# Optimization experiments

Hardware: AMD Instinct MI355X
Metric: run time of the kernel (lower is better)

## Reference

```python
import jax, jax.numpy as jnp
import numpy as np

B, S, D = 2, 400, 512  # batch, seq (src == tgt for self-attention), dim; attn_hidden=0 so d == D


def setup_inputs() -> dict:
    key = jax.random.key(0)
    ks = jax.random.split(key, 9)
    inv = 1.0 / np.sqrt(D)
    return {
        "input": jax.random.normal(ks[0], (B, S, D), jnp.float32),
        "memory_bank": jax.random.normal(ks[1], (B, S, D), jnp.float32),
        # lengths in [S//2, S], guaranteed >= 2 so no row is fully masked
        "memory_lengths": jax.random.randint(ks[2], (B,), S // 2, S + 1, jnp.int32),
        "Wq": jax.random.normal(ks[3], (D, D), jnp.float32) * inv,   # linear_query.weight^T
        "bq": jax.random.normal(ks[4], (D,), jnp.float32) * inv,      # linear_query.bias
        "Wc": jax.random.normal(ks[5], (D, D), jnp.float32) * inv,   # linear_context.weight^T
        "v": jax.random.normal(ks[6], (D,), jnp.float32) * inv,       # v.weight (d -> 1)
        "Wout": jax.random.normal(ks[7], (2 * D, D), jnp.float32) * inv,  # linear_out.weight^T
        "bout": jax.random.normal(ks[8], (D,), jnp.float32) * inv,
    }


def reference(input, memory_bank, memory_lengths, Wq, bq, Wc, v, Wout, bout):
    b, s, d = memory_bank.shape
    # Bahdanau/mlp score: v^T tanh(Wq q + b + Wc h)
    wq = jnp.einsum("btd,de->bte", input, Wq) + bq            # [B,T,d]
    uh = jnp.einsum("bsd,de->bse", memory_bank, Wc)           # [B,S,d]
    wquh = jnp.tanh(wq[:, :, None, :] + uh[:, None, :, :])    # [B,T,S,d] big intermediate
    scores = jnp.einsum("btse,e->bts", wquh, v)               # [B,T,S]
    # padding mask (j < length) with self position masked out on the diagonal
    pos = jnp.arange(s)
    key_mask = pos[None, :] < memory_lengths[:, None]         # [B,S]
    mask = key_mask[:, None, :] & (pos[:, None] != pos[None, :])  # [B,T,S]
    scores = jnp.where(mask, scores, -jnp.inf)
    align = jax.nn.softmax(scores, axis=2)                    # [B,T,S]
    c = jnp.einsum("bts,bsd->btd", align, memory_bank)        # context [B,T,D]
    concat_c = jnp.concatenate([c, input], axis=2)            # [B,T,2D]
    attn_h = jnp.einsum("btf,fd->btd", concat_c, Wout) + bout # [B,T,D]
    # mlp variant: no sigmoid gating
    return attn_h.transpose(1, 0, 2), align.transpose(1, 0, 2)  # [T,B,D], [T,B,S]
```

## Files before the change

kernel.cpp:

```cpp
#include <hip/hip_runtime.h>
#include <math.h>

#define BB 2
#define SS 400
#define DD 512
#define TWO_LOG2E 2.8853900817779268f

#if __has_builtin(__builtin_amdgcn_exp2f)
#define EXP2F(x) __builtin_amdgcn_exp2f(x)
#else
#define EXP2F(x) exp2f(x)
#endif
#define RCPF(x) __builtin_amdgcn_rcpf(x)

#define EAOFF 0
#define MOFF 409600
#define EB4OFF 819200
#define XOFF 1228800

typedef __bf16 bf16x8 __attribute__((ext_vector_type(8)));
typedef float floatx16 __attribute__((ext_vector_type(16)));

__global__ __launch_bounds__(256) void k0_all(
    const float* __restrict__ Wq, const float* __restrict__ Wc,
    const float* __restrict__ Wout, const float* __restrict__ input,
    const float* __restrict__ mbk, unsigned short* __restrict__ wt,
    unsigned short* __restrict__ ahi, unsigned short* __restrict__ alo)
{
    const int gid = blockIdx.x;
    if (gid < 1024) {
        const int g   = gid >> 9;
        const int rem = gid & 511;
        const int k0  = (rem & 15) * 32;
        const int n0  = (rem >> 4) * 32;

        __shared__ float tile[32][33];
        const int nn  = threadIdx.x & 31;
        const int kk0 = threadIdx.x >> 5;
        const int n   = n0 + nn;

        #pragma unroll
        for (int p = 0; p < 4; ++p) {
            const int k = k0 + kk0 + p * 8;
            float val;
            if (n0 < 512) val = (g ? Wc : Wq)[(size_t)k * 512 + n];
            else          val = Wout[((size_t)(g ? k : 512 + k)) * 512 + (n - 512)];
            tile[kk0 + p * 8][nn] = val;
        }
        __syncthreads();

        const int kc = threadIdx.x & 31;
        #pragma unroll
        for (int p = 0; p < 4; ++p) {
            const int nl = (threadIdx.x >> 5) + p * 8;
            const __bf16 h = (__bf16)tile[kc][nl];
            wt[((size_t)(g * 1024 + n0 + nl)) * 512 + k0 + kc] =
                __builtin_bit_cast(unsigned short, h);
        }
    } else {
        const int cid = gid - 1024;
        const int g   = (cid >= 400) ? 1 : 0;
        const int i4  = (cid - g * 400) * 256 + threadIdx.x;
        const float4 a = ((const float4*)(g ? mbk : input))[i4];
        ushort4 h, l;
        #pragma unroll
        for (int j = 0; j < 4; ++j) {
            const float av = (&a.x)[j];
            const __bf16 hh = (__bf16)av;
            (&h.x)[j] = __builtin_bit_cast(unsigned short, hh);
            const __bf16 ll = (__bf16)(av - (float)hh);
            (&l.x)[j] = __builtin_bit_cast(unsigned short, ll);
        }
        ((ushort4*)(ahi + (size_t)g * 409600))[i4] = h;
        ((ushort4*)(alo + (size_t)g * 409600))[i4] = l;
    }
}

__global__ __launch_bounds__(64) void k1_mfma(
    const unsigned short* __restrict__ ahi, const unsigned short* __restrict__ alo,
    const unsigned short* __restrict__ wt, const float* __restrict__ bq,
    const float* __restrict__ bout, float* __restrict__ ws,
    float* __restrict__ out0)
{
    const int lane = threadIdx.x;
    const int mt   = blockIdx.x;
    const int np   = blockIdx.y;
    const int g    = blockIdx.z;
    const int m    = lane & 31;
    const int kh   = lane >> 5;
    const int n0   = np * 64;

    const size_t arow = ((size_t)g * 800 + mt * 32 + m) * 512 + kh * 8;
    const unsigned short* __restrict__ ah = ahi + arow;
    const unsigned short* __restrict__ al = alo + arow;
    const unsigned short* __restrict__ w0 =
        wt + ((size_t)(g * 1024 + n0 + m)) * 512 + kh * 8;
    const unsigned short* __restrict__ w1 = w0 + (size_t)32 * 512;

    floatx16 acc0h, acc0l, acc1h, acc1l;
    #pragma unroll
    for (int i = 0; i < 16; ++i) { acc0h[i] = 0.f; acc0l[i] = 0.f;
                                   acc1h[i] = 0.f; acc1l[i] = 0.f; }

    #pragma unroll 4
    for (int ks = 0; ks < 32; ++ks) {
        const bf16x8 va0 = *(const bf16x8*)(ah + ks * 16);
        const bf16x8 va1 = *(const bf16x8*)(al + ks * 16);
        const bf16x8 bh0 = *(const bf16x8*)(w0 + ks * 16);
        const bf16x8 bh1 = *(const bf16x8*)(w1 + ks * 16);

        acc0h = __builtin_amdgcn_mfma_f32_32x32x16_bf16(va0, bh0, acc0h, 0, 0, 0);
        acc0l = __builtin_amdgcn_mfma_f32_32x32x16_bf16(va1, bh0, acc0l, 0, 0, 0);
        acc1h = __builtin_amdgcn_mfma_f32_32x32x16_bf16(va0, bh1, acc1h, 0, 0, 0);
        acc1l = __builtin_amdgcn_mfma_f32_32x32x16_bf16(va1, bh1, acc1l, 0, 0, 0);
    }

    const floatx16 c0 = acc0h + acc0l;
    const floatx16 c1 = acc1h + acc1l;
    const int rbase = kh * 4;

    #pragma unroll
    for (int r = 0; r < 16; ++r) {
        const int row  = (r & 3) + 8 * (r >> 2) + rbase;
        const int grow = mt * 32 + row;
        const int bi   = (grow >= SS) ? 1 : 0;
        const int rl   = grow - bi * SS;
        #pragma unroll
        for (int u = 0; u < 2; ++u) {
            const float val  = u ? c1[r] : c0[r];
            const int   gcol = n0 + u * 32 + m;
            if (g == 0) {
                if (gcol < 512) {
                    ws[EAOFF + (size_t)grow * 512 + gcol] =
                        EXP2F(TWO_LOG2E * (val + bq[gcol]));
                } else {
                    const int d = gcol - 512;
                    out0[((size_t)(rl * BB + bi)) * 512 + d] = val + bout[d];
                }
            } else {
                if (gcol < 512) {
                    ws[EB4OFF + (size_t)((bi * 128 + (gcol >> 2)) * SS + rl) * 4
                       + (gcol & 3)] = EXP2F(TWO_LOG2E * val);
                } else {
                    ws[MOFF + (size_t)grow * 512 + (gcol - 512)] = val;
                }
            }
        }
    }
}

__global__ __launch_bounds__(512) void k2_attn(
    const float* __restrict__ ws, const float* __restrict__ v,
    const int* __restrict__ lens, float* __restrict__ out1,
    float* __restrict__ out0)
{
    const int tp = blockIdx.x;
    const int b  = blockIdx.y;
    const int t0 = tp * 2;
    const int t1 = t0 + 1;
    const int tid = threadIdx.x;
    const int s   = tid;
    const int sidx = (s < SS) ? s : 0;
    const int len  = lens[b];

    __shared__ float lal[SS][2];
    __shared__ float wred0[8], wred1[8];

    const float* __restrict__ ea0p = ws + EAOFF + (size_t)(b * SS + t0) * 512;
    const float* __restrict__ ea1p = ea0p + 512;

    const float4* __restrict__ eb4 =
        (const float4*)(ws + EB4OFF) + (size_t)b * 128 * SS + sidx;

    float acc0 = 0.f, acc1 = 0.f;
    #pragma unroll 4
    for (int e4 = 0; e4 < 128; ++e4) {
        const float4 eb  = eb4[(size_t)e4 * SS];
        const float4 vv  = *(const float4*)(v    + e4 * 4);
        const float4 ea0 = *(const float4*)(ea0p + e4 * 4);
        const float4 ea1 = *(const float4*)(ea1p + e4 * 4);
        {
            const float d0 = fmaf(ea0.x, eb.x, 1.f);
            const float d1 = fmaf(ea0.y, eb.y, 1.f);
            const float d2 = fmaf(ea0.z, eb.z, 1.f);
            const float d3 = fmaf(ea0.w, eb.w, 1.f);
            const float d01 = d0 * d1, d23 = d2 * d3;
            const float n01 = fmaf(vv.x, d1, vv.y * d0);
            const float n23 = fmaf(vv.z, d3, vv.w * d2);
            const float num = fmaf(n01, d23, n23 * d01);
            acc0 = fmaf(num, RCPF(d01 * d23), acc0);
        }
        {
            const float d0 = fmaf(ea1.x, eb.x, 1.f);
            const float d1 = fmaf(ea1.y, eb.y, 1.f);
            const float d2 = fmaf(ea1.z, eb.z, 1.f);
            const float d3 = fmaf(ea1.w, eb.w, 1.f);
            const float d01 = d0 * d1, d23 = d2 * d3;
            const float n01 = fmaf(vv.x, d1, vv.y * d0);
            const float n23 = fmaf(vv.z, d3, vv.w * d2);
            const float num = fmaf(n01, d23, n23 * d01);
            acc1 = fmaf(num, RCPF(d01 * d23), acc1);
        }
    }

    const bool v0 = (s < SS) && (s < len) && (s != t0);
    const bool v1 = (s < SS) && (s < len) && (s != t1);
    const float sc0 = v0 ? -2.f * acc0 : -INFINITY;
    const float sc1 = v1 ? -2.f * acc1 : -INFINITY;

    const int wid  = tid >> 6;
    const int lane = tid & 63;

    float m0 = sc0, m1 = sc1;
    #pragma unroll
    for (int off = 32; off > 0; off >>= 1) {
        m0 = fmaxf(m0, __shfl_xor(m0, off));
        m1 = fmaxf(m1, __shfl_xor(m1, off));
    }
    if (lane == 0) { wred0[wid] = m0; wred1[wid] = m1; }
    __syncthreads();
    float mx0 = wred0[0], mx1 = wred1[0];
    #pragma unroll
    for (int w = 1; w < 8; ++w) {
        mx0 = fmaxf(mx0, wred0[w]);
        mx1 = fmaxf(mx1, wred1[w]);
    }
    __syncthreads();

    const float p0 = v0 ? __expf(sc0 - mx0) : 0.f;
    const float p1 = v1 ? __expf(sc1 - mx1) : 0.f;
    float s0v = p0, s1v = p1;
    #pragma unroll
    for (int off = 32; off > 0; off >>= 1) {
        s0v += __shfl_xor(s0v, off);
        s1v += __shfl_xor(s1v, off);
    }
    if (lane == 0) { wred0[wid] = s0v; wred1[wid] = s1v; }
    __syncthreads();
    float tot0 = wred0[0], tot1 = wred1[0];
    #pragma unroll
    for (int w = 1; w < 8; ++w) { tot0 += wred0[w]; tot1 += wred1[w]; }
    const float inv0 = RCPF(tot0);
    const float inv1 = RCPF(tot1);

    if (s < SS) {
        const float a0 = p0 * inv0;
        const float a1 = p1 * inv1;
        out1[((size_t)(t0 * BB) + b) * SS + s] = a0;
        out1[((size_t)(t1 * BB) + b) * SS + s] = a1;
        lal[s][0] = a0;
        lal[s][1] = a1;
    }
    __syncthreads();

    const float* __restrict__ Mb = ws + MOFF + (size_t)b * SS * DD;
    const int d = tid;
    float c0a = 0.f, c0b = 0.f, c1a = 0.f, c1b = 0.f;
    #pragma unroll 4
    for (int sp = 0; sp < SS; sp += 2) {
        const float mv0 = Mb[(size_t)sp * DD + d];
        const float mv1 = Mb[(size_t)(sp + 1) * DD + d];
        const float2 a0 = *(const float2*)&lal[sp][0];
        const float2 a1 = *(const float2*)&lal[sp + 1][0];
        c0a = fmaf(a0.x, mv0, c0a);
        c1a = fmaf(a0.y, mv0, c1a);
        c0b = fmaf(a1.x, mv1, c0b);
        c1b = fmaf(a1.y, mv1, c1b);
    }
    const size_t o0 = ((size_t)(t0 * BB) + b) * DD + d;
    const size_t o1 = ((size_t)(t1 * BB) + b) * DD + d;
    out0[o0] += c0a + c0b;
    out0[o1] += c1a + c1b;
}

extern "C" void kernel_launch(void* const* d_in, const int* in_sizes, int n_in,
                              void* d_out, int out_size, void* d_ws, size_t ws_size,
                              hipStream_t stream)
{
    const float* input = (const float*)d_in[0];
    const float* mbk   = (const float*)d_in[1];
    const int*   lens  = (const int*)d_in[2];
    const float* Wq    = (const float*)d_in[3];
    const float* bq    = (const float*)d_in[4];
    const float* Wc    = (const float*)d_in[5];
    const float* v     = (const float*)d_in[6];
    const float* Wout  = (const float*)d_in[7];
    const float* bout  = (const float*)d_in[8];

    float* out0 = (float*)d_out;
    float* out1 = out0 + (size_t)BB * SS * DD;
    float* ws   = (float*)d_ws;
    unsigned short* x16 = (unsigned short*)(ws + XOFF);
    unsigned short* wt  = x16;
    unsigned short* ahi = x16 + 1048576;
    unsigned short* alo = ahi + 819200;

    hipLaunchKernelGGL(k0_all, dim3(1824), dim3(256), 0, stream,
                       Wq, Wc, Wout, input, mbk, wt, ahi, alo);
    hipLaunchKernelGGL(k1_mfma, dim3(25, 16, 2), dim3(64), 0, stream,
                       ahi, alo, wt, bq, bout, ws, out0);
    hipLaunchKernelGGL(k2_attn, dim3(200, 2), dim3(512), 0, stream,
                       ws, v, lens, out1, out0);
}
```

Baseline: 145.0 us.

## Split attention score and context reductions across two half-blocks of threads

The attention kernel grows to 1024 threads. Two groups of 512 threads each compute half of the feature dimension of the score, and the partial sums are combined through shared memory. Score work is skipped for key positions at or beyond the sequence length, and the context accumulation only loops up to the length, with its s-range also split between the two halves. This raises parallelism per block and removes padded work, at the cost of extra barriers, more shared memory and tighter register pressure under the 1024-thread launch bound.

New measurement: 155.2 us. +7.0%, slower.

```diff
diff --git a/kernel.cpp b/kernel.cpp
--- a/kernel.cpp
+++ b/kernel.cpp
@@ -149,7 +149,7 @@
     }
 }
 
-__global__ __launch_bounds__(512) void k2_attn(
+__global__ __launch_bounds__(1024, 2) void k2_attn(
     const float* __restrict__ ws, const float* __restrict__ v,
     const int* __restrict__ lens, float* __restrict__ out1,
     float* __restrict__ out0)
@@ -159,12 +159,14 @@
     const int t0 = tp * 2;
     const int t1 = t0 + 1;
     const int tid = threadIdx.x;
-    const int s   = tid;
+    const int h   = tid >> 9;
+    const int s   = tid & 511;
     const int sidx = (s < SS) ? s : 0;
     const int len  = lens[b];
 
+    __shared__ float pacc[2][512];
     __shared__ float lal[SS][2];
-    __shared__ float wred0[8], wred1[8];
+    __shared__ float wredm0[8], wredm1[8], wreds0[8], wreds1[8];
 
     const float* __restrict__ ea0p = ws + EAOFF + (size_t)(b * SS + t0) * 512;
     const float* __restrict__ ea1p = ea0p + 512;
@@ -173,91 +175,109 @@
         (const float4*)(ws + EB4OFF) + (size_t)b * 128 * SS + sidx;
 
     float acc0 = 0.f, acc1 = 0.f;
-    #pragma unroll 4
-    for (int e4 = 0; e4 < 128; ++e4) {
-        const float4 eb  = eb4[(size_t)e4 * SS];
-        const float4 vv  = *(const float4*)(v    + e4 * 4);
-        const float4 ea0 = *(const float4*)(ea0p + e4 * 4);
-        const float4 ea1 = *(const float4*)(ea1p + e4 * 4);
-        {
-            const float d0 = fmaf(ea0.x, eb.x, 1.f);
-            const float d1 = fmaf(ea0.y, eb.y, 1.f);
-            const float d2 = fmaf(ea0.z, eb.z, 1.f);
-            const float d3 = fmaf(ea0.w, eb.w, 1.f);
-            const float d01 = d0 * d1, d23 = d2 * d3;
-            const float n01 = fmaf(vv.x, d1, vv.y * d0);
-            const float n23 = fmaf(vv.z, d3, vv.w * d2);
-            const float num = fmaf(n01, d23, n23 * d01);
-            acc0 = fmaf(num, RCPF(d01 * d23), acc0);
-        }
-        {
-            const float d0 = fmaf(ea1.x, eb.x, 1.f);
-            const float d1 = fmaf(ea1.y, eb.y, 1.f);
-            const float d2 = fmaf(ea1.z, eb.z, 1.f);
-            const float d3 = fmaf(ea1.w, eb.w, 1.f);
-            const float d01 = d0 * d1, d23 = d2 * d3;
-            const float n01 = fmaf(vv.x, d1, vv.y * d0);
-            const float n23 = fmaf(vv.z, d3, vv.w * d2);
-            const float num = fmaf(n01, d23, n23 * d01);
-            acc1 = fmaf(num, RCPF(d01 * d23), acc1);
-        }
-    }
-
-    const bool v0 = (s < SS) && (s < len) && (s != t0);
-    const bool v1 = (s < SS) && (s < len) && (s != t1);
-    const float sc0 = v0 ? -2.f * acc0 : -INFINITY;
-    const float sc1 = v1 ? -2.f * acc1 : -INFINITY;
+    if (s < len) {
+        const int e4b = h * 64;
+        #pragma unroll 4
+        for (int e4 = e4b; e4 < e4b + 64; ++e4) {
+            const float4 eb  = eb4[(size_t)e4 * SS];
+            const float4 vv  = *(const float4*)(v    + e4 * 4);
+            const float4 ea0 = *(const float4*)(ea0p + e4 * 4);
+            const float4 ea1 = *(const float4*)(ea1p + e4 * 4);
+            {
+                const float d0 = fmaf(ea0.x, eb.x, 1.f);
+                const float d1 = fmaf(ea0.y, eb.y, 1.f);
+                const float d2 = fmaf(ea0.z, eb.z, 1.f);
+                const float d3 = fmaf(ea0.w, eb.w, 1.f);
+                const float d01 = d0 * d1, d23 = d2 * d3;
+                const float n01 = fmaf(vv.x, d1, vv.y * d0);
+                const float n23 = fmaf(vv.z, d3, vv.w * d2);
+                const float num = fmaf(n01, d23, n23 * d01);
+                acc0 = fmaf(num, RCPF(d01 * d23), acc0);
+            }
+            {
+                const float d0 = fmaf(ea1.x, eb.x, 1.f);
+                const float d1 = fmaf(ea1.y, eb.y, 1.f);
+                const float d2 = fmaf(ea1.z, eb.z, 1.f);
+                const float d3 = fmaf(ea1.w, eb.w, 1.f);
+                const float d01 = d0 * d1, d23 = d2 * d3;
+                const float n01 = fmaf(vv.x, d1, vv.y * d0);
+                const float n23 = fmaf(vv.z, d3, vv.w * d2);
+                const float num = fmaf(n01, d23, n23 * d01);
+                acc1 = fmaf(num, RCPF(d01 * d23), acc1);
+            }
+        }
+    }
+    if (h == 1) { pacc[0][s] = acc0; pacc[1][s] = acc1; }
+    __syncthreads();
 
     const int wid  = tid >> 6;
     const int lane = tid & 63;
 
-    float m0 = sc0, m1 = sc1;
-    #pragma unroll
-    for (int off = 32; off > 0; off >>= 1) {
-        m0 = fmaxf(m0, __shfl_xor(m0, off));
-        m1 = fmaxf(m1, __shfl_xor(m1, off));
-    }
-    if (lane == 0) { wred0[wid] = m0; wred1[wid] = m1; }
-    __syncthreads();
-    float mx0 = wred0[0], mx1 = wred1[0];
-    #pragma unroll
-    for (int w = 1; w < 8; ++w) {
-        mx0 = fmaxf(mx0, wred0[w]);
-        mx1 = fmaxf(mx1, wred1[w]);
-    }
-    __syncthreads();
-
-    const float p0 = v0 ? __expf(sc0 - mx0) : 0.f;
-    const float p1 = v1 ? __expf(sc1 - mx1) : 0.f;
-    float s0v = p0, s1v = p1;
-    #pragma unroll
-    for (int off = 32; off > 0; off >>= 1) {
-        s0v += __shfl_xor(s0v, off);
-        s1v += __shfl_xor(s1v, off);
-    }
-    if (lane == 0) { wred0[wid] = s0v; wred1[wid] = s1v; }
-    __syncthreads();
-    float tot0 = wred0[0], tot1 = wred1[0];
-    #pragma unroll
-    for (int w = 1; w < 8; ++w) { tot0 += wred0[w]; tot1 += wred1[w]; }
-    const float inv0 = RCPF(tot0);
-    const float inv1 = RCPF(tot1);
-
-    if (s < SS) {
-        const float a0 = p0 * inv0;
-        const float a1 = p1 * inv1;
-        out1[((size_t)(t0 * BB) + b) * SS + s] = a0;
-        out1[((size_t)(t1 * BB) + b) * SS + s] = a1;
-        lal[s][0] = a0;
-        lal[s][1] = a1;
+    bool  v0 = false, v1 = false;
+    float sc0 = -INFINITY, sc1 = -INFINITY;
+    if (h == 0) {
+        acc0 += pacc[0][s];
+        acc1 += pacc[1][s];
+        v0 = (s < SS) && (s < len) && (s != t0);
+        v1 = (s < SS) && (s < len) && (s != t1);
+        sc0 = v0 ? -2.f * acc0 : -INFINITY;
+        sc1 = v1 ? -2.f * acc1 : -INFINITY;
+
+        float m0 = sc0, m1 = sc1;
+        #pragma unroll
+        for (int off = 32; off > 0; off >>= 1) {
+            m0 = fmaxf(m0, __shfl_xor(m0, off));
+            m1 = fmaxf(m1, __shfl_xor(m1, off));
+        }
+        if (lane == 0) { wredm0[wid] = m0; wredm1[wid] = m1; }
+    }
+    __syncthreads();
+
+    float p0 = 0.f, p1 = 0.f;
+    if (h == 0) {
+        float mx0 = wredm0[0], mx1 = wredm1[0];
+        #pragma unroll
+        for (int w = 1; w < 8; ++w) {
+            mx0 = fmaxf(mx0, wredm0[w]);
+            mx1 = fmaxf(mx1, wredm1[w]);
+        }
+        p0 = v0 ? __expf(sc0 - mx0) : 0.f;
+        p1 = v1 ? __expf(sc1 - mx1) : 0.f;
+        float s0v = p0, s1v = p1;
+        #pragma unroll
+        for (int off = 32; off > 0; off >>= 1) {
+            s0v += __shfl_xor(s0v, off);
+            s1v += __shfl_xor(s1v, off);
+        }
+        if (lane == 0) { wreds0[wid] = s0v; wreds1[wid] = s1v; }
+    }
+    __syncthreads();
+
+    if (h == 0) {
+        float tot0 = wreds0[0], tot1 = wreds1[0];
+        #pragma unroll
+        for (int w = 1; w < 8; ++w) { tot0 += wreds0[w]; tot1 += wreds1[w]; }
+        const float inv0 = RCPF(tot0);
+        const float inv1 = RCPF(tot1);
+        if (s < SS) {
+            const float a0 = p0 * inv0;
+            const float a1 = p1 * inv1;
+            out1[((size_t)(t0 * BB) + b) * SS + s] = a0;
+            out1[((size_t)(t1 * BB) + b) * SS + s] = a1;
+            lal[s][0] = a0;
+            lal[s][1] = a1;
+        }
     }
     __syncthreads();
 
     const float* __restrict__ Mb = ws + MOFF + (size_t)b * SS * DD;
-    const int d = tid;
+    const int d    = s;
+    const int sbeg = h * 200;
+    const int send = h ? len : 200;
     float c0a = 0.f, c0b = 0.f, c1a = 0.f, c1b = 0.f;
+    int sp = sbeg;
     #pragma unroll 4
-    for (int sp = 0; sp < SS; sp += 2) {
+    for (; sp + 2 <= send; sp += 2) {
         const float mv0 = Mb[(size_t)sp * DD + d];
         const float mv1 = Mb[(size_t)(sp + 1) * DD + d];
         const float2 a0 = *(const float2*)&lal[sp][0];
@@ -267,10 +287,20 @@
         c0b = fmaf(a1.x, mv1, c0b);
         c1b = fmaf(a1.y, mv1, c1b);
     }
-    const size_t o0 = ((size_t)(t0 * BB) + b) * DD + d;
-    const size_t o1 = ((size_t)(t1 * BB) + b) * DD + d;
-    out0[o0] += c0a + c0b;
-    out0[o1] += c1a + c1b;
+    if (sp < send) {
+        const float mv0 = Mb[(size_t)sp * DD + d];
+        const float2 a0 = *(const float2*)&lal[sp][0];
+        c0a = fmaf(a0.x, mv0, c0a);
+        c1a = fmaf(a0.y, mv0, c1a);
+    }
+    const float ct0 = c0a + c0b;
+    const float ct1 = c1a + c1b;
+    if (h == 1) { pacc[0][d] = ct0; pacc[1][d] = ct1; }
+    __syncthreads();
+    if (h == 0) {
+        out0[((size_t)(t0 * BB) + b) * DD + d] += ct0 + pacc[0][d];
+        out0[((size_t)(t1 * BB) + b) * DD + d] += ct1 + pacc[1][d];
+    }
 }
 
 extern "C" void kernel_launch(void* const* d_in, const int* in_sizes, int n_in,
@@ -299,6 +329,6 @@
                        Wq, Wc, Wout, input, mbk, wt, ahi, alo);
     hipLaunchKernelGGL(k1_mfma, dim3(25, 16, 2), dim3(64), 0, stream,
                        ahi, alo, wt, bq, bout, ws, out0);
-    hipLaunchKernelGGL(k2_attn, dim3(200, 2), dim3(512), 0, stream,
+    hipLaunchKernelGGL(k2_attn, dim3(200, 2), dim3(1024), 0, stream,
                        ws, v, lens, out1, out0);
 }
```

## Split attention score kernel over feature halves with separate softmax/context kernel

Applied to the files above, without the earlier changes.

Splits the fused score+softmax+context kernel into a score kernel that partitions the 512-wide feature reduction into two halves across a new grid dimension, writing partial scores to workspace. A second kernel sums the two partials, then does masking, softmax and the context accumulation. This doubles the number of blocks for the compute-heavy score phase to raise GPU occupancy, at the cost of an extra launch and a workspace round trip for partial scores.

Result: no change. 143.7 us (-0.9%).

```diff
diff --git a/kernel.cpp b/kernel.cpp
--- a/kernel.cpp
+++ b/kernel.cpp
@@ -17,6 +17,7 @@
 #define MOFF 409600
 #define EB4OFF 819200
 #define XOFF 1228800
+#define SPOFF 2572288
 
 typedef __bf16 bf16x8 __attribute__((ext_vector_type(8)));
 typedef float floatx16 __attribute__((ext_vector_type(16)));
@@ -149,32 +150,28 @@
     }
 }
 
-__global__ __launch_bounds__(512) void k2_attn(
+__global__ __launch_bounds__(512) void k2a_score(
     const float* __restrict__ ws, const float* __restrict__ v,
-    const int* __restrict__ lens, float* __restrict__ out1,
-    float* __restrict__ out0)
+    float* __restrict__ sp)
 {
     const int tp = blockIdx.x;
     const int b  = blockIdx.y;
+    const int eh = blockIdx.z;
     const int t0 = tp * 2;
     const int t1 = t0 + 1;
     const int tid = threadIdx.x;
     const int s   = tid;
     const int sidx = (s < SS) ? s : 0;
-    const int len  = lens[b];
-
-    __shared__ float lal[SS][2];
-    __shared__ float wred0[8], wred1[8];
 
     const float* __restrict__ ea0p = ws + EAOFF + (size_t)(b * SS + t0) * 512;
     const float* __restrict__ ea1p = ea0p + 512;
-
     const float4* __restrict__ eb4 =
         (const float4*)(ws + EB4OFF) + (size_t)b * 128 * SS + sidx;
 
     float acc0 = 0.f, acc1 = 0.f;
+    const int e4b = eh * 64;
     #pragma unroll 4
-    for (int e4 = 0; e4 < 128; ++e4) {
+    for (int e4 = e4b; e4 < e4b + 64; ++e4) {
         const float4 eb  = eb4[(size_t)e4 * SS];
         const float4 vv  = *(const float4*)(v    + e4 * 4);
         const float4 ea0 = *(const float4*)(ea0p + e4 * 4);
@@ -203,6 +200,32 @@
         }
     }
 
+    const size_t base = ((size_t)(eh * 2 + b)) * 400;
+    sp[(base + t0) * 512 + s] = acc0;
+    sp[(base + t1) * 512 + s] = acc1;
+}
+
+__global__ __launch_bounds__(512) void k2b_sm(
+    const float* __restrict__ ws, const float* __restrict__ sp,
+    const int* __restrict__ lens, float* __restrict__ out1,
+    float* __restrict__ out0)
+{
+    const int tp = blockIdx.x;
+    const int b  = blockIdx.y;
+    const int t0 = tp * 2;
+    const int t1 = t0 + 1;
+    const int tid = threadIdx.x;
+    const int s   = tid;
+    const int len  = lens[b];
+
+    __shared__ float lal[SS][2];
+    __shared__ float wred0[8], wred1[8];
+
+    const size_t b0 = ((size_t)(0 * 2 + b)) * 400;
+    const size_t b1 = ((size_t)(1 * 2 + b)) * 400;
+    const float acc0 = sp[(b0 + t0) * 512 + s] + sp[(b1 + t0) * 512 + s];
+    const float acc1 = sp[(b0 + t1) * 512 + s] + sp[(b1 + t1) * 512 + s];
+
     const bool v0 = (s < SS) && (s < len) && (s != t0);
     const bool v1 = (s < SS) && (s < len) && (s != t1);
     const float sc0 = v0 ? -2.f * acc0 : -INFINITY;
@@ -257,11 +280,11 @@
     const int d = tid;
     float c0a = 0.f, c0b = 0.f, c1a = 0.f, c1b = 0.f;
     #pragma unroll 4
-    for (int sp = 0; sp < SS; sp += 2) {
-        const float mv0 = Mb[(size_t)sp * DD + d];
-        const float mv1 = Mb[(size_t)(sp + 1) * DD + d];
-        const float2 a0 = *(const float2*)&lal[sp][0];
-        const float2 a1 = *(const float2*)&lal[sp + 1][0];
+    for (int sp2 = 0; sp2 < SS; sp2 += 2) {
+        const float mv0 = Mb[(size_t)sp2 * DD + d];
+        const float mv1 = Mb[(size_t)(sp2 + 1) * DD + d];
+        const float2 a0 = *(const float2*)&lal[sp2][0];
+        const float2 a1 = *(const float2*)&lal[sp2 + 1][0];
         c0a = fmaf(a0.x, mv0, c0a);
         c1a = fmaf(a0.y, mv0, c1a);
         c0b = fmaf(a1.x, mv1, c0b);
@@ -294,11 +317,14 @@
     unsigned short* wt  = x16;
     unsigned short* ahi = x16 + 1048576;
     unsigned short* alo = ahi + 819200;
+    float* sp = ws + SPOFF;
 
     hipLaunchKernelGGL(k0_all, dim3(1824), dim3(256), 0, stream,
                        Wq, Wc, Wout, input, mbk, wt, ahi, alo);
     hipLaunchKernelGGL(k1_mfma, dim3(25, 16, 2), dim3(64), 0, stream,
                        ahi, alo, wt, bq, bout, ws, out0);
-    hipLaunchKernelGGL(k2_attn, dim3(200, 2), dim3(512), 0, stream,
-                       ws, v, lens, out1, out0);
-}
+    hipLaunchKernelGGL(k2a_score, dim3(200, 2, 2), dim3(512), 0, stream,
+                       ws, v, sp);
+    hipLaunchKernelGGL(k2b_sm, dim3(200, 2), dim3(512), 0, stream,
+                       ws, sp, lens, out1, out0);
+}
```
